# Kernel tuning notes

Measured on AMD Instinct MI355X. Metric: run time of the kernel, lower is better.

## Reference

```python
import jax, jax.numpy as jnp
import numpy as np

# Fixed-step Dormand-Prince RK45 (dopri5) over t in [0, 1].
# torchdiffeq's dopri5 is adaptive; an adaptive while-loop is not
# reverse-differentiable in JAX, so we use the same dopri5 tableau with a
# fixed step count, which reproduces the per-step math exactly.
N_STEPS = 64

# dopri5 Butcher tableau (a-matrix rows; b = 5th-order weights = row a7)
A21 = 1/5
A31, A32 = 3/40, 9/40
A41, A42, A43 = 44/45, -56/15, 32/9
A51, A52, A53, A54 = 19372/6561, -25360/2187, 64448/6561, -212/729
A61, A62, A63, A64, A65 = 9017/3168, -355/33, 46732/5247, 49/176, -5103/18656
B1, B3, B4, B5, B6 = 35/384, 500/1113, 125/192, -2187/6784, 11/84


def setup_inputs() -> dict:
    key = jax.random.key(0)
    ks = jax.random.split(key, 7)
    data_dim, hidden_dim, batch = 512, 1024, 4096
    s1 = 1.0 / np.sqrt(data_dim)
    s2 = 1.0 / np.sqrt(hidden_dim)
    return {
        "x":  jax.random.normal(ks[0], (batch, data_dim), jnp.float32),
        "W1": jax.random.normal(ks[1], (hidden_dim, data_dim), jnp.float32) * s1,
        "b1": jax.random.normal(ks[2], (hidden_dim,), jnp.float32) * s1,
        "W2": jax.random.normal(ks[3], (hidden_dim, hidden_dim), jnp.float32) * s2,
        "b2": jax.random.normal(ks[4], (hidden_dim,), jnp.float32) * s2,
        "W3": jax.random.normal(ks[5], (data_dim, hidden_dim), jnp.float32) * s2,
        "b3": jax.random.normal(ks[6], (data_dim,), jnp.float32) * s2,
    }


def reference(x, W1, b1, W2, b2, W3, b3):
    def f(y):  # ODEFunc MLP: fc1 -> relu -> fc2 -> relu -> fc3 (autonomous)
        h = jax.nn.relu(y @ W1.T + b1)
        h = jax.nn.relu(h @ W2.T + b2)
        return h @ W3.T + b3

    h = jnp.float32(1.0 / N_STEPS)

    def step(y, _):
        k1 = f(y)
        k2 = f(y + h * (A21 * k1))
        k3 = f(y + h * (A31 * k1 + A32 * k2))
        k4 = f(y + h * (A41 * k1 + A42 * k2 + A43 * k3))
        k5 = f(y + h * (A51 * k1 + A52 * k2 + A53 * k3 + A54 * k4))
        k6 = f(y + h * (A61 * k1 + A62 * k2 + A63 * k3 + A64 * k4 + A65 * k5))
        y_next = y + h * (B1 * k1 + B3 * k3 + B4 * k4 + B5 * k5 + B6 * k6)
        return y_next, None

    y_final, _ = jax.lax.scan(step, x, None, length=N_STEPS)
    return y_final
```

## Files before the change

kernel.cpp:

```cpp
#include <hip/hip_runtime.h>
#include <hip/hip_bf16.h>
#include <stdint.h>
#include <stddef.h>

using bf16_t = __hip_bfloat16;
typedef __attribute__((ext_vector_type(8))) short short8;
typedef __attribute__((ext_vector_type(4))) float f32x4;

__device__ __forceinline__ void gload_lds16(void* lds, const void* g) {
  __builtin_amdgcn_global_load_lds(
      (const __attribute__((address_space(1))) unsigned int*)g,
      (__attribute__((address_space(3))) unsigned int*)lds,
      16, 0, 0);
}

template<int MODE>
__device__ __forceinline__ void gemm_core(
    const bf16_t* __restrict__ A, const bf16_t* __restrict__ B,
    const float* __restrict__ bias,
    bf16_t* __restrict__ obf,
    bf16_t* __restrict__ aux,
    bf16_t* __restrict__ vout,
    float* __restrict__ yf_out,
    const float* __restrict__ y_in,
    const bf16_t* __restrict__ p0, const bf16_t* __restrict__ p1,
    const bf16_t* __restrict__ p2, const bf16_t* __restrict__ p3,
    float c0, float c1, float c2, float c3, float ccur, int hinit,
    int M, int N, int K, int lgx)
{
  __shared__ __align__(16) bf16_t As[2][64 * 64];
  __shared__ __align__(16) bf16_t Bs[2][64 * 64];

  const int t    = threadIdx.x;
  const int lane = t & 63;
  const int wid  = t >> 6;
  const int wm   = wid >> 1;
  const int wn   = wid & 1;

  const int nwg = gridDim.x, bid = blockIdx.x;
  const int swz = (bid & 7) * (nwg >> 3) + (bid >> 3);
  const int gxm = (1 << lgx) - 1;
  const int bx  = swz & gxm;
  const int by  = swz >> lgx;
  const int bn0 = bx * 64, bm0 = by * 64;

  const bf16_t* Ag = A + (size_t)bm0 * K;
  const bf16_t* Bg = B + (size_t)bn0 * K;

  f32x4 acc[2][2] = {};

  auto stage = [&](int b, int kt) {
    const int k0 = kt * 64;
#pragma unroll
    for (int r = 0; r < 2; ++r) {
      int ch  = t + r * 256;
      int row = ch >> 3, s = ch & 7;
      int sl  = s ^ (row & 7);
      gload_lds16(&As[b][ch * 8], Ag + (size_t)row * K + k0 + sl * 8);
    }
#pragma unroll
    for (int r = 0; r < 2; ++r) {
      int ch  = t + r * 256;
      int row = ch >> 3, s = ch & 7;
      int sl  = s ^ (row & 7);
      gload_lds16(&Bs[b][ch * 8], Bg + (size_t)row * K + k0 + sl * 8);
    }
  };

  const int nt = K >> 6;
  stage(0, 0);

  const int ro = lane & 15;
  const int ks = lane >> 4;

  for (int tt = 0; tt < nt; ++tt) {
    const int c = tt & 1;
    asm volatile("s_waitcnt vmcnt(0)" ::: "memory");
    __builtin_amdgcn_s_barrier();
    asm volatile("" ::: "memory");
    if (tt + 1 < nt) stage(c ^ 1, tt + 1);

#pragma unroll
    for (int kk = 0; kk < 2; ++kk) {
      short8 af[2], bfr[2];
      const int slot = kk * 4 + ks;
#pragma unroll
      for (int mi = 0; mi < 2; ++mi) {
        int row = wm * 32 + mi * 16 + ro;
        int ch  = row * 8 + (slot ^ (row & 7));
        af[mi]  = *(const short8*)&As[c][ch * 8];
      }
#pragma unroll
      for (int ni = 0; ni < 2; ++ni) {
        int row = wn * 32 + ni * 16 + ro;
        int ch  = row * 8 + (slot ^ (row & 7));
        bfr[ni] = *(const short8*)&Bs[c][ch * 8];
      }
      __builtin_amdgcn_s_setprio(1);
#pragma unroll
      for (int mi = 0; mi < 2; ++mi)
#pragma unroll
        for (int ni = 0; ni < 2; ++ni)
          acc[mi][ni] = __builtin_amdgcn_mfma_f32_16x16x32_bf16(
              af[mi], bfr[ni], acc[mi][ni], 0, 0, 0);
      __builtin_amdgcn_s_setprio(0);
    }
  }

  const int rb = bm0 + wm * 32;
  const int cb = bn0 + wn * 32;
#pragma unroll
  for (int mi = 0; mi < 2; ++mi) {
#pragma unroll
    for (int ni = 0; ni < 2; ++ni) {
      const int col = cb + ni * 16 + ro;
      const float bv = bias ? bias[col] : 0.f;
#pragma unroll
      for (int r = 0; r < 4; ++r) {
        const int row = rb + mi * 16 + (lane >> 4) * 4 + r;
        const size_t idx = (size_t)row * N + col;
        const float a = acc[mi][ni][r];
        if (MODE == 0) {
          float v = fmaxf(a + bv, 0.f);
          obf[idx] = __float2bfloat16(v);
          if (aux) {
            float hs = ccur * v + (hinit ? 0.f : __bfloat162float(aux[idx]));
            aux[idx] = __float2bfloat16(hs);
          }
        } else if (MODE == 1) {
          vout[idx] = __float2bfloat16(a);
          float u = __bfloat162float(aux[idx]) + ccur * a + bv;
          if (p0) u += c0 * __bfloat162float(p0[idx]);
          if (p1) u += c1 * __bfloat162float(p1[idx]);
          if (p2) u += c2 * __bfloat162float(p2[idx]);
          if (p3) u += c3 * __bfloat162float(p3[idx]);
          obf[idx] = __float2bfloat16(fmaxf(u, 0.f));
        } else if (MODE == 2) {
          aux[idx] = __float2bfloat16(a);
          obf[idx] = __float2bfloat16(fmaxf(a + bv, 0.f));
        } else if (MODE == 3) {
          obf[idx] = __float2bfloat16(a);
        } else {
          float z = y_in[idx] + a + ccur * bv;
          yf_out[idx] = z;
          obf[idx] = __float2bfloat16(z);
        }
      }
    }
  }
}

#define GARGS                                                               \
    const bf16_t* A, const bf16_t* B, const float* bias, bf16_t* obf,       \
    bf16_t* aux, bf16_t* vout, float* yf_out, const float* y_in,            \
    const bf16_t* p0, const bf16_t* p1, const bf16_t* p2, const bf16_t* p3, \
    float c0, float c1, float c2, float c3, float ccur, int hinit,          \
    int M, int N, int K, int lgx
#define GPASS A,B,bias,obf,aux,vout,yf_out,y_in,p0,p1,p2,p3,c0,c1,c2,c3,ccur,hinit,M,N,K,lgx

extern "C" __global__ void __launch_bounds__(256, 4) gmid(GARGS) { gemm_core<0>(GPASS); }
extern "C" __global__ void __launch_bounds__(256, 4) gvst(GARGS) { gemm_core<1>(GPASS); }
extern "C" __global__ void __launch_bounds__(256, 4) gyw1(GARGS) { gemm_core<2>(GPASS); }
extern "C" __global__ void __launch_bounds__(256, 4) gw13(GARGS) { gemm_core<3>(GPASS); }
extern "C" __global__ void __launch_bounds__(256, 4) gyup(GARGS) { gemm_core<4>(GPASS); }

extern "C" __global__ void init_all(
    const float* __restrict__ x,
    const float* __restrict__ W1, const float* __restrict__ W2,
    const float* __restrict__ W3,
    const float* __restrict__ b1, const float* __restrict__ b3,
    bf16_t* __restrict__ W1b, bf16_t* __restrict__ W2b,
    bf16_t* __restrict__ W3b, bf16_t* __restrict__ W3Tb,
    float* __restrict__ y, bf16_t* __restrict__ yb,
    float* __restrict__ bS2, float* __restrict__ bS3, float* __restrict__ bS4,
    float* __restrict__ bS5, float* __restrict__ bS6,
    float s2, float s3, float s4, float s5, float s6)
{
  const int gt = blockIdx.x * blockDim.x + threadIdx.x;
  const int gs = gridDim.x * blockDim.x;
  auto cvt4 = [&](const float* in, bf16_t* outp, int n) {
    for (int i = gt * 4; i < n; i += gs * 4) {
      float4 v = *(const float4*)(in + i);
      bf16_t o[4] = {__float2bfloat16(v.x), __float2bfloat16(v.y),
                     __float2bfloat16(v.z), __float2bfloat16(v.w)};
      *(uint64_t*)(outp + i) = *(uint64_t*)o;
    }
  };
  cvt4(W1, W1b, 1024 * 512);
  cvt4(W2, W2b, 1024 * 1024);
  cvt4(W3, W3b, 512 * 1024);
  for (int i = gt; i < 512 * 1024; i += gs) {
    int d = i >> 10, j = i & 1023;
    W3Tb[(size_t)j * 512 + d] = __float2bfloat16(W3[i]);
  }
  for (int i = gt * 4; i < 4096 * 512; i += gs * 4) {
    float4 v = *(const float4*)(x + i);
    *(float4*)(y + i) = v;
    bf16_t o[4] = {__float2bfloat16(v.x), __float2bfloat16(v.y),
                   __float2bfloat16(v.z), __float2bfloat16(v.w)};
    *(uint64_t*)(yb + i) = *(uint64_t*)o;
  }
  if (gt < 1024) {
    float c13 = 0.f;
    const float* wr = W1 + (size_t)gt * 512;
    for (int d = 0; d < 512; ++d) c13 += b3[d] * wr[d];
    const float bb = b1[gt];
    bS2[gt] = bb + s2 * c13;
    bS3[gt] = bb + s3 * c13;
    bS4[gt] = bb + s4 * c13;
    bS5[gt] = bb + s5 * c13;
    bS6[gt] = bb + s6 * c13;
  }
}

extern "C" void kernel_launch(void* const* d_in, const int* in_sizes, int n_in,
                              void* d_out, int out_size, void* d_ws, size_t ws_size,
                              hipStream_t stream)
{
  const float* x  = (const float*)d_in[0];
  const float* W1 = (const float*)d_in[1];
  const float* b1 = (const float*)d_in[2];
  const float* W2 = (const float*)d_in[3];
  const float* b2 = (const float*)d_in[4];
  const float* W3 = (const float*)d_in[5];
  const float* b3 = (const float*)d_in[6];

  constexpr int BATCH = 4096, DATA = 512, HID = 1024;

  char* ws = (char*)d_ws;
  size_t off = 0;
  auto alloc = [&](size_t bytes) -> void* {
    off = (off + 255) & ~(size_t)255;
    void* p = ws + off;
    off += bytes;
    return p;
  };
  const size_t nyd = (size_t)BATCH * DATA;
  const size_t nh  = (size_t)BATCH * HID;

  float*  y    = (float*)alloc(nyd * 4);
  bf16_t* yb   = (bf16_t*)alloc(nyd * 2);
  bf16_t* h1b  = (bf16_t*)alloc(nh * 2);
  bf16_t* h2b  = (bf16_t*)alloc(nh * 2);
  bf16_t* yw1b = (bf16_t*)alloc(nh * 2);
  bf16_t* hsumb= (bf16_t*)alloc(nh * 2);
  bf16_t* v1   = (bf16_t*)alloc(nh * 2);
  bf16_t* v2   = (bf16_t*)alloc(nh * 2);
  bf16_t* v3   = (bf16_t*)alloc(nh * 2);
  bf16_t* v4   = (bf16_t*)alloc(nh * 2);
  bf16_t* v5   = (bf16_t*)alloc(nh * 2);
  bf16_t* W1b  = (bf16_t*)alloc((size_t)HID * DATA * 2);
  bf16_t* W2b  = (bf16_t*)alloc((size_t)HID * HID * 2);
  bf16_t* W3b  = (bf16_t*)alloc((size_t)DATA * HID * 2);
  bf16_t* W3Tb = (bf16_t*)alloc((size_t)HID * DATA * 2);
  bf16_t* W13b = (bf16_t*)alloc((size_t)HID * HID * 2);
  float*  bS2  = (float*)alloc(HID * 4);
  float*  bS3  = (float*)alloc(HID * 4);
  float*  bS4  = (float*)alloc(HID * 4);
  float*  bS5  = (float*)alloc(HID * 4);
  float*  bS6  = (float*)alloc(HID * 4);

  const double hh = 1.0 / 64.0;
  const float hA21 = (float)(hh * (1.0/5.0));
  const float hA31 = (float)(hh * (3.0/40.0)),    hA32 = (float)(hh * (9.0/40.0));
  const float hA41 = (float)(hh * (44.0/45.0)),   hA42 = (float)(hh * (-56.0/15.0)),
              hA43 = (float)(hh * (32.0/9.0));
  const float hA51 = (float)(hh * (19372.0/6561.0)),  hA52 = (float)(hh * (-25360.0/2187.0)),
              hA53 = (float)(hh * (64448.0/6561.0)),  hA54 = (float)(hh * (-212.0/729.0));
  const float hA61 = (float)(hh * (9017.0/3168.0)),   hA62 = (float)(hh * (-355.0/33.0)),
              hA63 = (float)(hh * (46732.0/5247.0)),  hA64 = (float)(hh * (49.0/176.0)),
              hA65 = (float)(hh * (-5103.0/18656.0));
  const float hB1 = (float)(hh * (35.0/384.0)),   hB3 = (float)(hh * (500.0/1113.0)),
              hB4 = (float)(hh * (125.0/192.0)),  hB5 = (float)(hh * (-2187.0/6784.0)),
              hB6 = (float)(hh * (11.0/84.0));
  const float s2 = hA21, s3 = hA31 + hA32, s4 = hA41 + hA42 + hA43,
              s5 = hA51 + hA52 + hA53 + hA54,
              s6 = hA61 + hA62 + hA63 + hA64 + hA65;

  init_all<<<2048, 256, 0, stream>>>(x, W1, W2, W3, b1, b3,
                                     W1b, W2b, W3b, W3Tb, y, yb,
                                     bS2, bS3, bS4, bS5, bS6,
                                     s2, s3, s4, s5, s6);

  const dim3 blk(256);
  const int gridN = (HID / 64) * (BATCH / 64);
  const int gridY = (DATA / 64) * (BATCH / 64);
  const int gridW = (HID / 64) * (HID / 64);

  gw13<<<gridW, blk, 0, stream>>>(
      W1b, W3Tb, nullptr, W13b, nullptr, nullptr, nullptr, nullptr,
      nullptr, nullptr, nullptr, nullptr, 0.f, 0.f, 0.f, 0.f, 0.f, 0,
      HID, HID, DATA, 4);

  auto G2 = [&](bf16_t* hs, float coef, int hinit) {
    gmid<<<gridN, blk, 0, stream>>>(
        h1b, W2b, b2, h2b, hs, nullptr, nullptr, nullptr,
        nullptr, nullptr, nullptr, nullptr,
        0.f, 0.f, 0.f, 0.f, coef, hinit, BATCH, HID, HID, 4);
  };
  auto V = [&](bf16_t* vo, const float* bS, float ccur,
               const bf16_t* q0, float cc0, const bf16_t* q1, float cc1,
               const bf16_t* q2, float cc2, const bf16_t* q3, float cc3) {
    gvst<<<gridN, blk, 0, stream>>>(
        h2b, W13b, bS, h1b, yw1b, vo, nullptr, nullptr,
        q0, q1, q2, q3, cc0, cc1, cc2, cc3, ccur, 0, BATCH, HID, HID, 4);
  };

  for (int step = 0; step < 64; ++step) {
    gyw1<<<gridN, blk, 0, stream>>>(
        yb, W1b, b1, h1b, yw1b, nullptr, nullptr, nullptr,
        nullptr, nullptr, nullptr, nullptr,
        0.f, 0.f, 0.f, 0.f, 0.f, 0, BATCH, HID, DATA, 4);
    G2(hsumb, hB1, 1);
    V(v1, bS2, hA21, nullptr,0,nullptr,0,nullptr,0,nullptr,0);
    G2(nullptr, 0.f, 0);
    V(v2, bS3, hA32, v1,hA31, nullptr,0,nullptr,0,nullptr,0);
    G2(hsumb, hB3, 0);
    V(v3, bS4, hA43, v1,hA41, v2,hA42, nullptr,0,nullptr,0);
    G2(hsumb, hB4, 0);
    V(v4, bS5, hA54, v1,hA51, v2,hA52, v3,hA53, nullptr,0);
    G2(hsumb, hB5, 0);
    V(v5, bS6, hA65, v1,hA61, v2,hA62, v3,hA63, v4,hA64);
    G2(hsumb, hB6, 0);
    float* yf = (step == 63) ? (float*)d_out : y;
    gyup<<<gridY, blk, 0, stream>>>(
        hsumb, W3b, b3, yb, nullptr, nullptr, yf, y,
        nullptr, nullptr, nullptr, nullptr,
        0.f, 0.f, 0.f, 0.f, (float)hh, 0, BATCH, DATA, HID, 3);
  }
}
```

Before: 17.50 ms.

## Fold per-step y update into a fused hsum@W13 first-layer GEMM

Instead of rebuilding y each step with a y-update GEMM and then recomputing y·W1 from scratch, the first-layer pre-activation is kept as an fp32 accumulator. Each step it is advanced with hsum_prev @ (W1·W3) plus a folded bias term. The running sum of hsum is also accumulated in fp32 and applied once at the end through a single W3 GEMM, with a small elementwise kernel adding the final step's contribution. This removes one GEMM launch per step and stops y being rounded to bf16 every step. In exchange it adds fp32 read-modify-write traffic on two activation-sized buffers, and the merged GEMM does the same FLOPs as the two it replaces.

```diff
diff --git a/kernel.cpp b/kernel.cpp
--- a/kernel.cpp
+++ b/kernel.cpp
@@ -21,6 +21,7 @@
     bf16_t* __restrict__ obf,
     bf16_t* __restrict__ aux,
     bf16_t* __restrict__ vout,
+    float* __restrict__ wacc,
     float* __restrict__ yf_out,
     const float* __restrict__ y_in,
     const bf16_t* __restrict__ p0, const bf16_t* __restrict__ p1,
@@ -129,21 +130,25 @@
           }
         } else if (MODE == 1) {
           vout[idx] = __float2bfloat16(a);
-          float u = __bfloat162float(aux[idx]) + ccur * a + bv;
+          float u = wacc[idx] + ccur * a + bv;
           if (p0) u += c0 * __bfloat162float(p0[idx]);
           if (p1) u += c1 * __bfloat162float(p1[idx]);
           if (p2) u += c2 * __bfloat162float(p2[idx]);
           if (p3) u += c3 * __bfloat162float(p3[idx]);
           obf[idx] = __float2bfloat16(fmaxf(u, 0.f));
         } else if (MODE == 2) {
-          aux[idx] = __float2bfloat16(a);
-          obf[idx] = __float2bfloat16(fmaxf(a + bv, 0.f));
+          wacc[idx]   = a;
+          yf_out[idx] = 0.f;
+          obf[idx]    = __float2bfloat16(fmaxf(a + bv, 0.f));
         } else if (MODE == 3) {
           obf[idx] = __float2bfloat16(a);
+        } else if (MODE == 4) {
+          yf_out[idx] = y_in[idx] + a + ccur * bv;
         } else {
-          float z = y_in[idx] + a + ccur * bv;
-          yf_out[idx] = z;
-          obf[idx] = __float2bfloat16(z);
+          float u = wacc[idx] + a + ccur * bv;
+          wacc[idx] = u;
+          yf_out[idx] += __bfloat162float(p0[idx]);
+          obf[idx] = __float2bfloat16(fmaxf(u + y_in[col], 0.f));
         }
       }
     }
@@ -152,17 +157,19 @@
 
 #define GARGS                                                               \
     const bf16_t* A, const bf16_t* B, const float* bias, bf16_t* obf,       \
-    bf16_t* aux, bf16_t* vout, float* yf_out, const float* y_in,            \
+    bf16_t* aux, bf16_t* vout, float* wacc, float* yf_out,                  \
+    const float* y_in,                                                      \
     const bf16_t* p0, const bf16_t* p1, const bf16_t* p2, const bf16_t* p3, \
     float c0, float c1, float c2, float c3, float ccur, int hinit,          \
     int M, int N, int K, int lgx
-#define GPASS A,B,bias,obf,aux,vout,yf_out,y_in,p0,p1,p2,p3,c0,c1,c2,c3,ccur,hinit,M,N,K,lgx
+#define GPASS A,B,bias,obf,aux,vout,wacc,yf_out,y_in,p0,p1,p2,p3,c0,c1,c2,c3,ccur,hinit,M,N,K,lgx
 
 extern "C" __global__ void __launch_bounds__(256, 4) gmid(GARGS) { gemm_core<0>(GPASS); }
 extern "C" __global__ void __launch_bounds__(256, 4) gvst(GARGS) { gemm_core<1>(GPASS); }
 extern "C" __global__ void __launch_bounds__(256, 4) gyw1(GARGS) { gemm_core<2>(GPASS); }
 extern "C" __global__ void __launch_bounds__(256, 4) gw13(GARGS) { gemm_core<3>(GPASS); }
-extern "C" __global__ void __launch_bounds__(256, 4) gyup(GARGS) { gemm_core<4>(GPASS); }
+extern "C" __global__ void __launch_bounds__(256, 4) gfin(GARGS) { gemm_core<4>(GPASS); }
+extern "C" __global__ void __launch_bounds__(256, 4) gs1v(GARGS) { gemm_core<5>(GPASS); }
 
 extern "C" __global__ void init_all(
     const float* __restrict__ x,
@@ -171,7 +178,8 @@
     const float* __restrict__ b1, const float* __restrict__ b3,
     bf16_t* __restrict__ W1b, bf16_t* __restrict__ W2b,
     bf16_t* __restrict__ W3b, bf16_t* __restrict__ W3Tb,
-    float* __restrict__ y, bf16_t* __restrict__ yb,
+    bf16_t* __restrict__ yb,
+    float* __restrict__ c13f,
     float* __restrict__ bS2, float* __restrict__ bS3, float* __restrict__ bS4,
     float* __restrict__ bS5, float* __restrict__ bS6,
     float s2, float s3, float s4, float s5, float s6)
@@ -189,27 +197,41 @@
   cvt4(W1, W1b, 1024 * 512);
   cvt4(W2, W2b, 1024 * 1024);
   cvt4(W3, W3b, 512 * 1024);
+  cvt4(x, (bf16_t*)yb, 4096 * 512);
   for (int i = gt; i < 512 * 1024; i += gs) {
     int d = i >> 10, j = i & 1023;
     W3Tb[(size_t)j * 512 + d] = __float2bfloat16(W3[i]);
-  }
-  for (int i = gt * 4; i < 4096 * 512; i += gs * 4) {
-    float4 v = *(const float4*)(x + i);
-    *(float4*)(y + i) = v;
-    bf16_t o[4] = {__float2bfloat16(v.x), __float2bfloat16(v.y),
-                   __float2bfloat16(v.z), __float2bfloat16(v.w)};
-    *(uint64_t*)(yb + i) = *(uint64_t*)o;
   }
   if (gt < 1024) {
     float c13 = 0.f;
     const float* wr = W1 + (size_t)gt * 512;
     for (int d = 0; d < 512; ++d) c13 += b3[d] * wr[d];
     const float bb = b1[gt];
+    c13f[gt] = c13;
     bS2[gt] = bb + s2 * c13;
     bS3[gt] = bb + s3 * c13;
     bS4[gt] = bb + s4 * c13;
     bS5[gt] = bb + s5 * c13;
     bS6[gt] = bb + s6 * c13;
+  }
+}
+
+extern "C" __global__ void ewfin(const float* __restrict__ Stot,
+                                 const bf16_t* __restrict__ hsum,
+                                 bf16_t* __restrict__ Stotb, int n)
+{
+  const int gt = blockIdx.x * blockDim.x + threadIdx.x;
+  const int gs = gridDim.x * blockDim.x;
+  for (int i = gt * 4; i < n; i += gs * 4) {
+    float4 s = *(const float4*)(Stot + i);
+    uint64_t hv = *(const uint64_t*)(hsum + i);
+    const bf16_t* hp = (const bf16_t*)&hv;
+    bf16_t o[4];
+    o[0] = __float2bfloat16(s.x + __bfloat162float(hp[0]));
+    o[1] = __float2bfloat16(s.y + __bfloat162float(hp[1]));
+    o[2] = __float2bfloat16(s.z + __bfloat162float(hp[2]));
+    o[3] = __float2bfloat16(s.w + __bfloat162float(hp[3]));
+    *(uint64_t*)(Stotb + i) = *(uint64_t*)o;
   }
 }
 
@@ -238,11 +260,12 @@
   const size_t nyd = (size_t)BATCH * DATA;
   const size_t nh  = (size_t)BATCH * HID;
 
-  float*  y    = (float*)alloc(nyd * 4);
   bf16_t* yb   = (bf16_t*)alloc(nyd * 2);
   bf16_t* h1b  = (bf16_t*)alloc(nh * 2);
   bf16_t* h2b  = (bf16_t*)alloc(nh * 2);
-  bf16_t* yw1b = (bf16_t*)alloc(nh * 2);
+  float*  yw1f = (float*)alloc(nh * 4);
+  float*  Stot = (float*)alloc(nh * 4);
+  bf16_t* Stotb= (bf16_t*)alloc(nh * 2);
   bf16_t* hsumb= (bf16_t*)alloc(nh * 2);
   bf16_t* v1   = (bf16_t*)alloc(nh * 2);
   bf16_t* v2   = (bf16_t*)alloc(nh * 2);
@@ -254,6 +277,7 @@
   bf16_t* W3b  = (bf16_t*)alloc((size_t)DATA * HID * 2);
   bf16_t* W3Tb = (bf16_t*)alloc((size_t)HID * DATA * 2);
   bf16_t* W13b = (bf16_t*)alloc((size_t)HID * HID * 2);
+  float*  c13f = (float*)alloc(HID * 4);
   float*  bS2  = (float*)alloc(HID * 4);
   float*  bS3  = (float*)alloc(HID * 4);
   float*  bS4  = (float*)alloc(HID * 4);
@@ -278,8 +302,8 @@
               s6 = hA61 + hA62 + hA63 + hA64 + hA65;
 
   init_all<<<2048, 256, 0, stream>>>(x, W1, W2, W3, b1, b3,
-                                     W1b, W2b, W3b, W3Tb, y, yb,
-                                     bS2, bS3, bS4, bS5, bS6,
+                                     W1b, W2b, W3b, W3Tb, yb,
+                                     c13f, bS2, bS3, bS4, bS5, bS6,
                                      s2, s3, s4, s5, s6);
 
   const dim3 blk(256);
@@ -288,13 +312,13 @@
   const int gridW = (HID / 64) * (HID / 64);
 
   gw13<<<gridW, blk, 0, stream>>>(
-      W1b, W3Tb, nullptr, W13b, nullptr, nullptr, nullptr, nullptr,
+      W1b, W3Tb, nullptr, W13b, nullptr, nullptr, nullptr, nullptr, nullptr,
       nullptr, nullptr, nullptr, nullptr, 0.f, 0.f, 0.f, 0.f, 0.f, 0,
       HID, HID, DATA, 4);
 
   auto G2 = [&](bf16_t* hs, float coef, int hinit) {
     gmid<<<gridN, blk, 0, stream>>>(
-        h1b, W2b, b2, h2b, hs, nullptr, nullptr, nullptr,
+        h1b, W2b, b2, h2b, hs, nullptr, nullptr, nullptr, nullptr,
         nullptr, nullptr, nullptr, nullptr,
         0.f, 0.f, 0.f, 0.f, coef, hinit, BATCH, HID, HID, 4);
   };
@@ -302,15 +326,22 @@
                const bf16_t* q0, float cc0, const bf16_t* q1, float cc1,
                const bf16_t* q2, float cc2, const bf16_t* q3, float cc3) {
     gvst<<<gridN, blk, 0, stream>>>(
-        h2b, W13b, bS, h1b, yw1b, vo, nullptr, nullptr,
+        h2b, W13b, bS, h1b, nullptr, vo, yw1f, nullptr, nullptr,
         q0, q1, q2, q3, cc0, cc1, cc2, cc3, ccur, 0, BATCH, HID, HID, 4);
   };
 
   for (int step = 0; step < 64; ++step) {
-    gyw1<<<gridN, blk, 0, stream>>>(
-        yb, W1b, b1, h1b, yw1b, nullptr, nullptr, nullptr,
-        nullptr, nullptr, nullptr, nullptr,
-        0.f, 0.f, 0.f, 0.f, 0.f, 0, BATCH, HID, DATA, 4);
+    if (step == 0) {
+      gyw1<<<gridN, blk, 0, stream>>>(
+          yb, W1b, b1, h1b, nullptr, nullptr, yw1f, Stot, nullptr,
+          nullptr, nullptr, nullptr, nullptr,
+          0.f, 0.f, 0.f, 0.f, 0.f, 0, BATCH, HID, DATA, 4);
+    } else {
+      gs1v<<<gridN, blk, 0, stream>>>(
+          hsumb, W13b, c13f, h1b, nullptr, nullptr, yw1f, Stot, b1,
+          hsumb, nullptr, nullptr, nullptr,
+          0.f, 0.f, 0.f, 0.f, (float)hh, 0, BATCH, HID, HID, 4);
+    }
     G2(hsumb, hB1, 1);
     V(v1, bS2, hA21, nullptr,0,nullptr,0,nullptr,0,nullptr,0);
     G2(nullptr, 0.f, 0);
@@ -322,10 +353,11 @@
     G2(hsumb, hB5, 0);
     V(v5, bS6, hA65, v1,hA61, v2,hA62, v3,hA63, v4,hA64);
     G2(hsumb, hB6, 0);
-    float* yf = (step == 63) ? (float*)d_out : y;
-    gyup<<<gridY, blk, 0, stream>>>(
-        hsumb, W3b, b3, yb, nullptr, nullptr, yf, y,
-        nullptr, nullptr, nullptr, nullptr,
-        0.f, 0.f, 0.f, 0.f, (float)hh, 0, BATCH, DATA, HID, 3);
-  }
-}
+  }
+
+  ewfin<<<1024, 256, 0, stream>>>(Stot, hsumb, Stotb, (int)nh);
+  gfin<<<gridY, blk, 0, stream>>>(
+      Stotb, W3b, b3, nullptr, nullptr, nullptr, nullptr, (float*)d_out, x,
+      nullptr, nullptr, nullptr, nullptr,
+      0.f, 0.f, 0.f, 0.f, 1.0f, 0, BATCH, DATA, HID, 3);
+}
```

New measurement: 17.68 ms. About the same (+1.1%).
